# Kernel tuning notes

Hardware: AMD Instinct MI355X
Metric: run time of the kernel (lower is better)

Reference implementation:

```python
import jax, jax.numpy as jnp
import numpy as np

N = 6144   # number of patches (bag size)
L = 1024   # input feature dim
D = 512    # GCN hidden dim
ALPHA = 0.4
THRESH = 0.5


def _layernorm(x, g, b):
    m = jnp.mean(x, axis=-1, keepdims=True)
    v = jnp.mean((x - m) ** 2, axis=-1, keepdims=True)
    return (x - m) / jnp.sqrt(v + 1e-5) * g + b


def _l1rows(x):
    # F.normalize(x, p=1): row-wise L1 normalize with eps=1e-12
    return x / jnp.maximum(jnp.sum(jnp.abs(x), axis=1, keepdims=True), 1e-12)


def _nonlin(x, w1, b1, g, bn, w2, b2):
    h = jax.nn.relu(_layernorm(x @ w1 + b1, g, bn))
    return h @ w2 + b2


def _gcn(x, adj, w, b, g, bn):
    # GraphConvolution: adj @ (x @ W) + bias, then LayerNorm + ReLU
    return jax.nn.relu(_layernorm(adj @ (x @ w) + b, g, bn))


def setup_inputs() -> dict:
    key = jax.random.key(0)
    ks = iter(jax.random.split(key, 64))

    def nrm(shape, s=0.02):
        return jax.random.normal(next(ks), shape, jnp.float32) * s

    inp = {
        'x_path': jax.random.normal(next(ks), (N, L), jnp.float32),
        'maps': jax.random.uniform(next(ks), (N, N), jnp.float32) * 0.1,
    }
    for pre in ['nl0', 'nl1']:
        inp[pre + '_w1'] = nrm((L, D)); inp[pre + '_b1'] = jnp.zeros((D,), jnp.float32)
        inp[pre + '_g'] = jnp.ones((D,), jnp.float32); inp[pre + '_bn'] = jnp.zeros((D,), jnp.float32)
        inp[pre + '_w2'] = nrm((D, D)); inp[pre + '_b2'] = jnp.zeros((D,), jnp.float32)
    for pre in ['gc0', 'gc1', 'gc2', 'ga0', 'ga1', 'ga2']:
        inp[pre + '_w'] = nrm((D, D)); inp[pre + '_b'] = jnp.zeros((D,), jnp.float32)
        inp[pre + '_g'] = jnp.ones((D,), jnp.float32); inp[pre + '_bn'] = jnp.zeros((D,), jnp.float32)
    inp['attn_wa'] = nrm((L, 256)); inp['attn_ba'] = jnp.zeros((256,), jnp.float32)
    inp['attn_wb'] = nrm((L, 256)); inp['attn_bb'] = jnp.zeros((256,), jnp.float32)
    inp['attn_wc'] = nrm((256, 1)); inp['attn_bc'] = jnp.zeros((1,), jnp.float32)
    inp['cls_w'] = nrm((L, 4), 0.001)
    inp['ln_g'] = jnp.ones((L,), jnp.float32); inp['ln_b'] = jnp.zeros((L,), jnp.float32)
    return inp


def reference(x_path, maps,
              nl0_w1, nl0_b1, nl0_g, nl0_bn, nl0_w2, nl0_b2,
              nl1_w1, nl1_b1, nl1_g, nl1_bn, nl1_w2, nl1_b2,
              gc0_w, gc0_b, gc0_g, gc0_bn,
              gc1_w, gc1_b, gc1_g, gc1_bn,
              gc2_w, gc2_b, gc2_g, gc2_bn,
              ga0_w, ga0_b, ga0_g, ga0_bn,
              ga1_w, ga1_b, ga1_g, ga1_bn,
              ga2_w, ga2_b, ga2_g, ga2_bn,
              attn_wa, attn_ba, attn_wb, attn_bb, attn_wc, attn_bc,
              cls_w, ln_g, ln_b):
    # cosine-similarity adjacency: L2-normalize rows, gram matrix, min-max, threshold
    xn = x_path / jnp.maximum(jnp.linalg.norm(x_path, axis=1, keepdims=True), 1e-12)
    cs = xn @ xn.T                                       # [N,N]
    cs = (cs - cs.min()) / (cs.max() - cs.min())
    cs = (cs >= THRESH).astype(jnp.float32)

    # gated attention (eval mode, no dropout): A = Wc (tanh(Wa x) * sigmoid(Wb x))
    a = jnp.tanh(x_path @ attn_wa + attn_ba)
    bg = jax.nn.sigmoid(x_path @ attn_wb + attn_bb)
    agg = (a * bg) @ attn_wc + attn_bc                   # [N,1]

    s = jax.nn.sigmoid(agg)
    aw = s * s.T                                         # outer product [N,N]
    aw = (aw - aw.min()) / (aw.max() - aw.min())
    aw = ALPHA + (1.0 - ALPHA) * aw + maps

    cs = _l1rows(cs)
    aw = _l1rows(aw)

    x0 = _nonlin(x_path, nl0_w1, nl0_b1, nl0_g, nl0_bn, nl0_w2, nl0_b2)
    x1 = _nonlin(x_path, nl1_w1, nl1_b1, nl1_g, nl1_bn, nl1_w2, nl1_b2)

    g1 = _gcn(x0, cs, gc0_w, gc0_b, gc0_g, gc0_bn)
    g1 = _gcn(g1, cs, gc1_w, gc1_b, gc1_g, gc1_bn)
    g1 = _gcn(g1, cs, gc2_w, gc2_b, gc2_g, gc2_bn)

    g2 = _gcn(x1, aw, ga0_w, ga0_b, ga0_g, ga0_bn)
    g2 = _gcn(g2, aw, ga1_w, ga1_b, ga1_g, ga1_bn)
    g2 = _gcn(g2, aw, ga2_w, ga2_b, ga2_g, ga2_bn)

    gcf = jnp.concatenate([g2, g1], axis=1)              # [N, 1024]

    n = x_path.shape[0]
    trans = (cs @ agg) / (n ** 0.5)                      # [N,1]
    fw = jax.nn.softmax(0.3 * trans + 0.7 * agg, axis=0) # softmax over patches
    pooled = fw.T @ gcf                                  # [1, 1024]
    pooled = _layernorm(pooled, ln_g, ln_b)

    logits = pooled @ cls_w                              # [1, 4]
    y_hat = jnp.argmax(logits, axis=1, keepdims=True)    # topk k=1 index
    hazards = jax.nn.sigmoid(logits)
    surv = jnp.cumprod(1.0 - hazards, axis=1)
    return hazards, surv, y_hat
```

## Files before the change

### kernel.cpp

```cpp
#include <hip/hip_runtime.h>

#define N_ 6144
#define L_ 1024
#define D_ 512
#define H_ 256
#define SPARSE_MAX 64u

typedef unsigned short u16;
typedef unsigned long long u64;
typedef __attribute__((ext_vector_type(4))) float f32x4;
typedef __attribute__((ext_vector_type(8))) short s16x8;
typedef __attribute__((ext_vector_type(4))) short s16x4;

__device__ __forceinline__ u16 f2b(float f){
  unsigned u = __float_as_uint(f);
  u += 0x7FFFu + ((u >> 16) & 1u);
  return (u16)(u >> 16);
}
__device__ __forceinline__ float b2f(u16 h){ return __uint_as_float(((unsigned)h) << 16); }
__device__ __forceinline__ unsigned fkey(float f){
  unsigned u = __float_as_uint(f);
  return (u & 0x80000000u) ? ~u : (u | 0x80000000u);
}
__device__ __forceinline__ float funkey(unsigned k){
  unsigned u = (k & 0x80000000u) ? (k & 0x7FFFFFFFu) : ~k;
  return __uint_as_float(u);
}
__device__ __forceinline__ float wave_sum(float v){
  #pragma unroll
  for(int o=32;o;o>>=1) v += __shfl_xor(v,o);
  return v;
}
__device__ __forceinline__ float wave_max(float v){
  #pragma unroll
  for(int o=32;o;o>>=1) v = fmaxf(v,__shfl_xor(v,o));
  return v;
}
__device__ __forceinline__ float wave_min(float v){
  #pragma unroll
  for(int o=32;o;o>>=1) v = fminf(v,__shfl_xor(v,o));
  return v;
}
__device__ __forceinline__ float blk_sum256(float v){
  __shared__ float sm[4];
  v = wave_sum(v);
  __syncthreads();
  if((threadIdx.x&63)==0) sm[threadIdx.x>>6]=v;
  __syncthreads();
  return sm[0]+sm[1]+sm[2]+sm[3];
}
__device__ __forceinline__ float blk_min256(float v){
  __shared__ float sm[4];
  v = wave_min(v);
  __syncthreads();
  if((threadIdx.x&63)==0) sm[threadIdx.x>>6]=v;
  __syncthreads();
  return fminf(fminf(sm[0],sm[1]),fminf(sm[2],sm[3]));
}
__device__ __forceinline__ float blk_max256(float v){
  __shared__ float sm[4];
  v = wave_max(v);
  __syncthreads();
  if((threadIdx.x&63)==0) sm[threadIdx.x>>6]=v;
  __syncthreads();
  return fmaxf(fmaxf(sm[0],sm[1]),fmaxf(sm[2],sm[3]));
}

template<int VW> __device__ __forceinline__ void waitv(){
  if constexpr(VW==8) asm volatile("s_waitcnt vmcnt(8)" ::: "memory");
  else if constexpr(VW==4) asm volatile("s_waitcnt vmcnt(4)" ::: "memory");
  else asm volatile("s_waitcnt vmcnt(0)" ::: "memory");
}

#define STG4(bb,k0) do{ \
  __builtin_amdgcn_global_load_lds((__attribute__((address_space(1))) void*)(gA0+(k0)), (__attribute__((address_space(3))) void*)(lds + (bb)*4096 + (wid<<9)),        16, 0, 0); \
  __builtin_amdgcn_global_load_lds((__attribute__((address_space(1))) void*)(gA1+(k0)), (__attribute__((address_space(3))) void*)(lds + (bb)*4096 + 2048 + (wid<<9)), 16, 0, 0); \
  __builtin_amdgcn_global_load_lds((__attribute__((address_space(1))) void*)(gB0+(k0)), (__attribute__((address_space(3))) void*)(lds + 12288 + (bb)*4096 + (wid<<9)),        16, 0, 0); \
  __builtin_amdgcn_global_load_lds((__attribute__((address_space(1))) void*)(gB1+(k0)), (__attribute__((address_space(3))) void*)(lds + 12288 + (bb)*4096 + 2048 + (wid<<9)), 16, 0, 0); \
}while(0)

template<int MODE>
__global__ __launch_bounds__(256) void gemm_bt(
  const u16* __restrict__ A, const u16* __restrict__ Bt,
  int M, int Nc, int K,
  u16* __restrict__ Cb, unsigned* __restrict__ mmx,
  const unsigned* __restrict__ gate)
{
  if (gate && gate[2] <= SPARSE_MAX) return;
  __shared__ __align__(16) u16 lds[3*4096*2];
  const int tid = threadIdx.x;
  const int wid = tid>>6, lane = tid&63;

  int m0, n0;
  if (MODE==1){
    int t = (int)blockIdx.x;
    t = (t&7)*147 + (t>>3);
    int i=0, rem=t;
    while (rem >= 48-i){ rem -= 48-i; ++i; }
    m0 = i<<7; n0 = (i+rem)<<7;
  } else {
    const int gx = gridDim.x;
    int lid = blockIdx.y*gx + blockIdx.x;
    const int nwg = gx*gridDim.y;
    if ((nwg & 7) == 0) {
      const int chunk = nwg >> 3;
      lid = (lid & 7)*chunk + (lid >> 3);
    }
    m0 = (lid/gx)<<7; n0 = (lid%gx)<<7;
  }
  const int wr = wid>>1, wc = wid&1;

  const int Klen = K / gridDim.z;
  const int kbeg = blockIdx.z * Klen;

  const int srow = (wid<<4) + (lane>>2);
  const int scol = (lane&3)<<3;
  const u16* gA0 = A  + (size_t)(m0+srow   )*K + scol;
  const u16* gA1 = A  + (size_t)(m0+srow+64)*K + scol;
  const u16* gB0 = Bt + (size_t)(n0+srow   )*K + scol;
  const u16* gB1 = Bt + (size_t)(n0+srow+64)*K + scol;

  f32x4 acc[4][4] = {};
  const int lr = lane&15, lk = (lane>>4)<<3;

  const int NIT = Klen>>5;
  STG4(0, kbeg);
  STG4(1, kbeg+32);
  STG4(2, kbeg+64);

  for (int it=0; it<NIT-2; ++it){
    const int b = it - (it/3)*3;
    waitv<8>();
    __builtin_amdgcn_s_barrier();
    const u16* baseA = lds + b*4096;
    const u16* baseB = lds + 12288 + b*4096;
    s16x8 af[4], bfr[4];
    #pragma unroll
    for(int m=0;m<4;m++) af[m]  = *(const s16x8*)(baseA + ((wr<<6)+(m<<4)+lr)*32 + lk);
    #pragma unroll
    for(int n=0;n<4;n++) bfr[n] = *(const s16x8*)(baseB + ((wc<<6)+(n<<4)+lr)*32 + lk);
    asm volatile("s_waitcnt lgkmcnt(0)" ::: "memory");
    __builtin_amdgcn_sched_barrier(0);
    __builtin_amdgcn_s_barrier();
    if (it+3 < NIT) STG4(b, kbeg + ((it+3)<<5));
    #pragma unroll
    for(int m=0;m<4;m++)
      #pragma unroll
      for(int n=0;n<4;n++)
        acc[m][n] = __builtin_amdgcn_mfma_f32_16x16x32_bf16(af[m], bfr[n], acc[m][n], 0,0,0);
  }
  {
    const int it = NIT-2; const int b = it - (it/3)*3;
    waitv<4>();
    __builtin_amdgcn_s_barrier();
    const u16* baseA = lds + b*4096;
    const u16* baseB = lds + 12288 + b*4096;
    s16x8 af[4], bfr[4];
    #pragma unroll
    for(int m=0;m<4;m++) af[m]  = *(const s16x8*)(baseA + ((wr<<6)+(m<<4)+lr)*32 + lk);
    #pragma unroll
    for(int n=0;n<4;n++) bfr[n] = *(const s16x8*)(baseB + ((wc<<6)+(n<<4)+lr)*32 + lk);
    #pragma unroll
    for(int m=0;m<4;m++)
      #pragma unroll
      for(int n=0;n<4;n++)
        acc[m][n] = __builtin_amdgcn_mfma_f32_16x16x32_bf16(af[m], bfr[n], acc[m][n], 0,0,0);
  }
  {
    const int it = NIT-1; const int b = it - (it/3)*3;
    waitv<0>();
    __builtin_amdgcn_s_barrier();
    const u16* baseA = lds + b*4096;
    const u16* baseB = lds + 12288 + b*4096;
    s16x8 af[4], bfr[4];
    #pragma unroll
    for(int m=0;m<4;m++) af[m]  = *(const s16x8*)(baseA + ((wr<<6)+(m<<4)+lr)*32 + lk);
    #pragma unroll
    for(int n=0;n<4;n++) bfr[n] = *(const s16x8*)(baseB + ((wc<<6)+(n<<4)+lr)*32 + lk);
    #pragma unroll
    for(int m=0;m<4;m++)
      #pragma unroll
      for(int n=0;n<4;n++)
        acc[m][n] = __builtin_amdgcn_mfma_f32_16x16x32_bf16(af[m], bfr[n], acc[m][n], 0,0,0);
  }

  float tmin = 3.0e38f, tmax = -3.0e38f;
  if (MODE==1){
    #pragma unroll
    for(int m=0;m<4;m++)
      #pragma unroll
      for(int n=0;n<4;n++){
        f32x4 v = acc[m][n];
        #pragma unroll
        for(int e=0;e<4;e++){ tmin = fminf(tmin,v[e]); tmax = fmaxf(tmax,v[e]); }
      }
  }

  __syncthreads();
  u16* lC = lds;
  {
    const int rb_l = (wr<<6) + ((lane>>4)<<2);
    const int cb_l = (wc<<6) + lr;
    #pragma unroll
    for(int m=0;m<4;m++)
      #pragma unroll
      for(int n=0;n<4;n++){
        f32x4 v = acc[m][n];
        #pragma unroll
        for(int e=0;e<4;e++)
          lC[(rb_l+(m<<4)+e)*128 + cb_l+(n<<4)] = f2b(v[e]);
      }
  }
  __syncthreads();
  u16* Cp = (MODE==0) ? (Cb + (size_t)blockIdx.z * M * Nc) : Cb;
  #pragma unroll
  for(int q=0;q<8;q++){
    int c = (q<<8) + tid;
    int r = c>>4, cc = (c&15)<<3;
    s16x8 v = *(const s16x8*)(lC + r*128 + cc);
    if (MODE==1)
      __builtin_nontemporal_store(v, (s16x8*)(Cp + (size_t)(m0+r)*Nc + n0 + cc));
    else
      *(s16x8*)(Cp + (size_t)(m0+r)*Nc + n0 + cc) = v;
  }

  if (MODE==1){
    tmin = wave_min(tmin); tmax = wave_max(tmax);
    __shared__ float rmn[4], rmx[4];
    if(lane==0){ rmn[wid]=tmin; rmx[wid]=tmax; }
    __syncthreads();
    if(tid==0){
      float mn=fminf(fminf(rmn[0],rmn[1]),fminf(rmn[2],rmn[3]));
      float mx=fmaxf(fmaxf(rmx[0],rmx[1]),fmaxf(rmx[2],rmx[3]));
      atomicMin(mmx+0, fkey(mn));
      atomicMax(mmx+1, fkey(mx));
    }
  }
}

__global__ __launch_bounds__(256) void mirror_lower(u16* __restrict__ C,
  const unsigned* __restrict__ gate)
{
  if (gate[2] <= SPARSE_MAX) return;
  int c0 = blockIdx.x<<5, r0 = blockIdx.y<<5;
  if ((r0>>7) >= (c0>>7)) return;
  __shared__ u16 t[32][33];
  int tx = threadIdx.x&31, ty = threadIdx.x>>5;
  #pragma unroll
  for(int i=0;i<32;i+=8) t[ty+i][tx] = C[(size_t)(r0+ty+i)*N_ + c0+tx];
  __syncthreads();
  #pragma unroll
  for(int i=0;i<32;i+=8)
    __builtin_nontemporal_store(t[tx][ty+i], C + (size_t)(c0+ty+i)*N_ + r0+tx);
}

struct TDesc { const float* src; u16* dst; int R; int C; int base; };
struct TDescs { TDesc d[12]; };
__global__ __launch_bounds__(256) void transpose_cast_multi(TDescs ds, int nd)
{
  int b = (int)blockIdx.x;
  int k = 0;
  for (int q=1;q<nd;q++) if (b >= ds.d[q].base) k = q;
  const float* src = ds.d[k].src;
  u16* dst = ds.d[k].dst;
  int R = ds.d[k].R, C = ds.d[k].C;
  int lt = b - ds.d[k].base;
  int tc = C>>5;
  int bx = lt % tc, by = lt / tc;
  __shared__ float t[32][33];
  int c0 = bx<<5, r0 = by<<5;
  int tx = threadIdx.x&31, ty = threadIdx.x>>5;
  #pragma unroll
  for(int i=0;i<32;i+=8) t[ty+i][tx] = src[(size_t)(r0+ty+i)*C + c0+tx];
  __syncthreads();
  #pragma unroll
  for(int i=0;i<32;i+=8) dst[(size_t)(c0+ty+i)*R + r0+tx] = f2b(t[tx][ty+i]);
}

__global__ __launch_bounds__(256) void transpose_sum_bf(
  const u16* __restrict__ src, size_t pstr, int nsp,
  u16* __restrict__ dst, int R, int C, const unsigned* __restrict__ gate)
{
  if (gate && gate[2] <= SPARSE_MAX) return;
  __shared__ float t[32][33];
  int c0 = blockIdx.x<<5, r0 = blockIdx.y<<5;
  int tx = threadIdx.x&31, ty = threadIdx.x>>5;
  #pragma unroll
  for(int i=0;i<32;i+=8){
    float v = 0;
    for(int p=0;p<nsp;p++)
      v += b2f(src[(size_t)p*pstr + (size_t)(r0+ty+i)*C + c0+tx]);
    t[ty+i][tx] = v;
  }
  __syncthreads();
  #pragma unroll
  for(int i=0;i<32;i+=8) dst[(size_t)(c0+ty+i)*R + r0+tx] = f2b(t[tx][ty+i]);
}

__global__ __launch_bounds__(256) void prep_x(const float* __restrict__ x,
  u16* __restrict__ xb, u16* __restrict__ xnb)
{
  int row = blockIdx.x, t = threadIdx.x;
  const float* p = x + (size_t)row*L_ + (t<<2);
  f32x4 v = *(const f32x4*)p;
  float ss = v[0]*v[0]+v[1]*v[1]+v[2]*v[2]+v[3]*v[3];
  float tot = blk_sum256(ss);
  float inv = 1.0f/fmaxf(sqrtf(tot), 1e-12f);
  u16* pb = xb  + (size_t)row*L_ + (t<<2);
  u16* pn = xnb + (size_t)row*L_ + (t<<2);
  #pragma unroll
  for(int k=0;k<4;k++){ pb[k]=f2b(v[k]); pn[k]=f2b(v[k]*inv); }
}

__global__ __launch_bounds__(256) void attn_epi(const u16* __restrict__ SPA,
  size_t pstr, int nsp,
  const float* __restrict__ ba, const float* __restrict__ bb,
  const float* __restrict__ wc, const float* __restrict__ bc,
  float* __restrict__ agg, float* __restrict__ s)
{
  int row = (blockIdx.x<<2) + (threadIdx.x>>6);
  int lane = threadIdx.x&63;
  float a[4]={0,0,0,0}, b[4]={0,0,0,0};
  for(int p=0;p<nsp;p++){
    s16x4 ua = *(const s16x4*)(SPA + (size_t)p*pstr + (size_t)row*1536 + (lane<<2));
    s16x4 ub = *(const s16x4*)(SPA + (size_t)p*pstr + (size_t)row*1536 + 256 + (lane<<2));
    #pragma unroll
    for(int j=0;j<4;j++){ a[j]+=b2f((u16)ua[j]); b[j]+=b2f((u16)ub[j]); }
  }
  float acc=0;
  #pragma unroll
  for(int j=0;j<4;j++){
    int h = (lane<<2)+j;
    float tv = tanhf(a[j]+ba[h]);
    float sg = 1.0f/(1.0f+expf(-(b[j]+bb[h])));
    acc += tv*sg*wc[h];
  }
  acc = wave_sum(acc);
  if(lane==0){
    float v = acc + bc[0];
    agg[row]=v;
    s[row]=1.0f/(1.0f+expf(-v));
  }
}

__global__ __launch_bounds__(256) void s_stats(const float* __restrict__ s, float* __restrict__ sc){
  int t=threadIdx.x;
  float mn=3e38f, mx=-3e38f;
  for(int i=t;i<N_;i+=256){ float v=s[i]; mn=fminf(mn,v); mx=fmaxf(mx,v); }
  float MN=blk_min256(mn);
  float MX=blk_max256(mx);
  if(t==0){ sc[0]=MN; sc[1]=MX; }
}

__global__ __launch_bounds__(256) void aw_write(const float* __restrict__ maps, const float* __restrict__ s,
  const float* __restrict__ sc, u16* __restrict__ awb)
{
  int i = blockIdx.x, t = threadIdx.x;
  float smin = sc[0], smax = sc[1];
  float mn = smin*smin, mx = smax*smax;
  float beta = 0.6f/(mx-mn);
  float c1 = 0.4f - beta*mn;
  float si = s[i];
  const float* mrow = maps + (size_t)i*N_;
  float mv[24];
  float part = 0;
  #pragma unroll
  for(int q=0;q<24;q++){
    int j = t + (q<<8);
    mv[q] = c1 + beta*si*s[j] + mrow[j];
    part += mv[q];
  }
  float r = blk_sum256(part);
  float inv = 1.0f/fmaxf(r, 1e-12f);
  u16* orow = awb + (size_t)i*N_;
  #pragma unroll
  for(int q=0;q<24;q++)
    __builtin_nontemporal_store(f2b(mv[q]*inv), orow + t + (q<<8));
}

__global__ __launch_bounds__(256) void ln_epi512(const u16* __restrict__ Y, size_t pstr, int nsp,
  int rs, int cbase,
  const float* __restrict__ ki,
  const float* __restrict__ bias, const float* __restrict__ g, const float* __restrict__ bn,
  u16* __restrict__ outb,
  const unsigned* __restrict__ gate)
{
  if (gate && gate[2] <= SPARSE_MAX) return;
  int row = (blockIdx.x<<2)+(threadIdx.x>>6);
  int lane = threadIdx.x&63;
  int c0 = lane<<3;
  float v[8] = {0,0,0,0,0,0,0,0};
  for(int p=0;p<nsp;p++){
    s16x8 u = *(const s16x8*)(Y + (size_t)p*pstr + (size_t)row*rs + cbase + c0);
    #pragma unroll
    for(int j=0;j<8;j++) v[j] += b2f((u16)u[j]);
  }
  float scale = ki ? (1.0f/ki[row]) : 1.0f;
  float sum=0, ssum=0;
  #pragma unroll
  for(int j=0;j<8;j++){ v[j] = v[j]*scale + bias[c0+j]; sum+=v[j]; ssum+=v[j]*v[j]; }
  sum = wave_sum(sum); ssum = wave_sum(ssum);
  float m = sum*(1.0f/D_);
  float var = ssum*(1.0f/D_) - m*m;
  float invsd = rsqrtf(var + 1e-5f);
  u16 ob[8];
  #pragma unroll
  for(int j=0;j<8;j++){
    float o = (v[j]-m)*invsd*g[c0+j] + bn[c0+j];
    o = fmaxf(o, 0.0f);
    ob[j] = f2b(o);
  }
  *(s16x8*)(outb + (size_t)row*D_ + c0) = *(s16x8*)ob;
}

__global__ __launch_bounds__(256) void ln_epi_proj(const u16* __restrict__ Y, size_t pstr, int nsp,
  const float* __restrict__ b1, const float* __restrict__ g1, const float* __restrict__ n1, u16* __restrict__ o1,
  const float* __restrict__ b0, const float* __restrict__ g0, const float* __restrict__ n0, u16* __restrict__ o0)
{
  const int sel = blockIdx.y;
  const int cbase = sel ? 512 : 1024;
  const float* bias = sel ? b0 : b1;
  const float* g    = sel ? g0 : g1;
  const float* bn   = sel ? n0 : n1;
  u16* outb         = sel ? o0 : o1;
  int row = (blockIdx.x<<2)+(threadIdx.x>>6);
  int lane = threadIdx.x&63;
  int c0 = lane<<3;
  float v[8] = {0,0,0,0,0,0,0,0};
  for(int p=0;p<nsp;p++){
    s16x8 u = *(const s16x8*)(Y + (size_t)p*pstr + (size_t)row*1536 + cbase + c0);
    #pragma unroll
    for(int j=0;j<8;j++) v[j] += b2f((u16)u[j]);
  }
  float sum=0, ssum=0;
  #pragma unroll
  for(int j=0;j<8;j++){ v[j] = v[j] + bias[c0+j]; sum+=v[j]; ssum+=v[j]*v[j]; }
  sum = wave_sum(sum); ssum = wave_sum(ssum);
  float m = sum*(1.0f/D_);
  float var = ssum*(1.0f/D_) - m*m;
  float invsd = rsqrtf(var + 1e-5f);
  u16 ob[8];
  #pragma unroll
  for(int j=0;j<8;j++){
    float o = (v[j]-m)*invsd*g[c0+j] + bn[c0+j];
    o = fmaxf(o, 0.0f);
    ob[j] = f2b(o);
  }
  *(s16x8*)(outb + (size_t)row*D_ + c0) = *(s16x8*)ob;
}

__global__ __launch_bounds__(256) void bias_cast(const u16* __restrict__ Y, size_t pstr, int nsp,
  const float* __restrict__ b, u16* __restrict__ outb)
{
  size_t idx = ((size_t)blockIdx.x*256 + threadIdx.x)<<3;
  float v[8] = {0,0,0,0,0,0,0,0};
  for(int p=0;p<nsp;p++){
    s16x8 u = *(const s16x8*)(Y + (size_t)p*pstr + idx);
    #pragma unroll
    for(int j=0;j<8;j++) v[j] += b2f((u16)u[j]);
  }
  int c = (int)(idx & (D_-1));
  u16 ob[8];
  #pragma unroll
  for(int k=0;k<8;k++) ob[k] = f2b(v[k]+b[c+k]);
  *(s16x8*)(outb+idx) = *(s16x8*)ob;
}

__global__ void init_k(unsigned* mmx){
  mmx[0]=0xFFFFFFFFu; mmx[1]=0u; mmx[2]=0u;
}

__global__ __launch_bounds__(256) void binarize_tri(const u16* __restrict__ csb,
  const unsigned* __restrict__ mmx, u64* __restrict__ bm)
{
  int i = blockIdx.x, t = threadIdx.x;
  int lane = t&63, w = t>>6;
  float mn = funkey(mmx[0]), mx = funkey(mmx[1]);
  float th = mn + 0.5f*(mx-mn);
  const u16* row = csb + (size_t)i*N_;
  u64* bmrow = bm + (size_t)i*96;
  const int w0 = i>>6;
  for (int wq = w0 + w; wq < 96; wq += 4){
    int j = (wq<<6) + lane;
    bool on = (j >= i) && (b2f(row[j]) >= th);
    u64 mask = __ballot(on);
    if (lane == 0){
      if (wq == w0) atomicOr((u64*)(bmrow+wq), mask);
      else bmrow[wq] = mask;
    }
    if (on && j > i)
      atomicOr((u64*)(bm + (size_t)j*96 + w0), 1ull << (i&63));
  }
}

__global__ __launch_bounds__(256) void binarize_fin(const u64* __restrict__ bm,
  unsigned* __restrict__ mmx, const float* __restrict__ agg,
  float* __restrict__ ki, float* __restrict__ z)
{
  int i = blockIdx.x, t = threadIdx.x;
  float cnt = 0, dot = 0;
  if (t < 96){
    u64 m = bm[(size_t)i*96 + t];
    cnt = (float)__popcll(m);
    while (m){
      int b = __ffsll((long long)m) - 1;
      m &= m - 1;
      dot += agg[(t<<6) + b];
    }
  }
  float k  = blk_sum256(cnt);
  float dt = blk_sum256(dot);
  if (t==0){
    ki[i] = k;
    float tr = dt/(k*sqrtf((float)N_));
    z[i] = 0.3f*tr + 0.7f*agg[i];
    if (k > (float)SPARSE_MAX)
      atomicMax(mmx+2, (unsigned)(k+0.5f));
  }
}

__global__ __launch_bounds__(256) void binarize_store(u16* __restrict__ csb,
  const unsigned* __restrict__ mmx)
{
  if (mmx[2] <= SPARSE_MAX) return;
  int i = blockIdx.x, t = threadIdx.x;
  float mn = funkey(mmx[0]), mx = funkey(mmx[1]);
  float th = mn + 0.5f*(mx-mn);
  u16* row = csb + (size_t)i*N_;
  #pragma unroll
  for(int q=0;q<24;q++){
    int j = t + (q<<8);
    row[j] = (b2f(row[j]) >= th) ? (u16)0x3F80 : (u16)0;
  }
}

__global__ __launch_bounds__(256) void gather_ln(const u64* __restrict__ bm,
  const u16* __restrict__ SPp, size_t pstr, int nsp,
  const unsigned* __restrict__ gate, const float* __restrict__ ki,
  const float* __restrict__ bias, const float* __restrict__ g, const float* __restrict__ bn,
  u16* __restrict__ outb)
{
  if (gate[2] > SPARSE_MAX) return;
  int i = blockIdx.x, t = threadIdx.x;
  __shared__ u64 wbuf[96];
  __shared__ u16 idx[SPARSE_MAX];
  __shared__ int nn_s;
  if (t < 96) wbuf[t] = bm[(size_t)i*96 + t];
  __syncthreads();
  if (t == 0){
    int nn = 0;
    for(int k=0;k<96;k++){
      u64 m = wbuf[k];
      while(m && nn < (int)SPARSE_MAX){
        int b = __ffsll((long long)m) - 1;
        m &= m - 1;
        idx[nn++] = (u16)((k<<6) + b);
      }
    }
    nn_s = nn;
  }
  __syncthreads();
  int nn = nn_s;
  float a0=0, a1=0;
  for(int k=0;k<nn;k++){
    size_t jb = (size_t)idx[k]*512;
    for(int p=0;p<nsp;p++){
      a0 += b2f(SPp[p*pstr + jb + t]);
      a1 += b2f(SPp[p*pstr + jb + t + 256]);
    }
  }
  float scale = 1.0f/ki[i];
  float v0 = a0*scale + bias[t];
  float v1 = a1*scale + bias[t+256];
  float sum  = blk_sum256(v0+v1);
  float ssum = blk_sum256(v0*v0+v1*v1);
  float m = sum*(1.0f/512.0f);
  float var = ssum*(1.0f/512.0f) - m*m;
  float inv = rsqrtf(var+1e-5f);
  float o0 = fmaxf((v0-m)*inv*g[t]+bn[t], 0.0f);
  float o1 = fmaxf((v1-m)*inv*g[t+256]+bn[t+256], 0.0f);
  outb[(size_t)i*512 + t]       = f2b(o0);
  outb[(size_t)i*512 + t + 256] = f2b(o1);
}

__global__ __launch_bounds__(1024) void softmax_prep(const float* __restrict__ z,
  float* __restrict__ e, float* __restrict__ sexp)
{
  int t = threadIdx.x;
  __shared__ float sm[16];
  float mx=-3e38f;
  for(int i=t;i<N_;i+=1024) mx=fmaxf(mx,z[i]);
  mx = wave_max(mx);
  if((t&63)==0) sm[t>>6]=mx;
  __syncthreads();
  float zm = sm[0];
  #pragma unroll
  for(int w=1;w<16;w++) zm=fmaxf(zm,sm[w]);
  __syncthreads();
  float sum=0;
  for(int i=t;i<N_;i+=1024){ float ee=expf(z[i]-zm); e[i]=ee; sum+=ee; }
  sum = wave_sum(sum);
  if((t&63)==0) sm[t>>6]=sum;
  __syncthreads();
  if(t==0){ float S=0; for(int w=0;w<16;w++) S+=sm[w]; *sexp=S; }
}

__global__ __launch_bounds__(256) void pooled_partial(const float* __restrict__ e,
  const u16* __restrict__ g2b, const u16* __restrict__ g1b, float* __restrict__ part)
{
  int b = blockIdx.x, t = threadIdx.x;
  float a0=0,a1=0,a2=0,a3=0;
  for(int r=0;r<192;r++){
    int row = b*192+r;
    float w = e[row];
    a0 += w * b2f(g2b[(size_t)row*D_ + t]);
    a1 += w * b2f(g2b[(size_t)row*D_ + t+256]);
    a2 += w * b2f(g1b[(size_t)row*D_ + t]);
    a3 += w * b2f(g1b[(size_t)row*D_ + t+256]);
  }
  part[(size_t)b*1024 + t]      = a0;
  part[(size_t)b*1024 + t+256]  = a1;
  part[(size_t)b*1024 + t+512]  = a2;
  part[(size_t)b*1024 + t+768]  = a3;
}

__global__ __launch_bounds__(1024) void final_k(const float* __restrict__ part, const float* __restrict__ sexp,
  const float* __restrict__ lng, const float* __restrict__ lnb,
  const float* __restrict__ clsw, float* __restrict__ out)
{
  int t = threadIdx.x;
  __shared__ float red[16];
  __shared__ float smv[1024];
  __shared__ float lgs[4];
  float p=0;
  for(int b=0;b<32;b++) p += part[b*1024 + t];
  p /= sexp[0];
  float w = wave_sum(p);
  if((t&63)==0) red[t>>6]=w;
  __syncthreads();
  float tot=0;
  #pragma unroll
  for(int i2=0;i2<16;i2++) tot+=red[i2];
  float m = tot*(1.0f/1024.0f);
  __syncthreads();
  float d = p-m;
  w = wave_sum(d*d);
  if((t&63)==0) red[t>>6]=w;
  __syncthreads();
  tot=0;
  #pragma unroll
  for(int i2=0;i2<16;i2++) tot+=red[i2];
  float var = tot*(1.0f/1024.0f);
  float y = d*rsqrtf(var+1e-5f)*lng[t] + lnb[t];
  smv[t]=y;
  __syncthreads();
  if(t<4){
    float lg=0;
    for(int j=0;j<1024;j++) lg += smv[j]*clsw[j*4+t];
    lgs[t]=lg;
  }
  __syncthreads();
  if(t==0){
    float h[4];
    int am=0; float best=lgs[0];
    #pragma unroll
    for(int c2=0;c2<4;c2++){ h[c2]=1.0f/(1.0f+expf(-lgs[c2])); if(lgs[c2]>best){best=lgs[c2];am=c2;} }
    float sv=1.0f;
    #pragma unroll
    for(int c2=0;c2<4;c2++){ out[c2]=h[c2]; sv*=(1.0f-h[c2]); out[4+c2]=sv; }
    out[8]=(float)am;
  }
}

extern "C" void kernel_launch(void* const* d_in, const int* in_sizes, int n_in,
                              void* d_out, int out_size, void* d_ws, size_t ws_size,
                              hipStream_t stream)
{
  const float* x_path =(const float*)d_in[0];
  const float* maps   =(const float*)d_in[1];
  const float* nl0_w1 =(const float*)d_in[2];
  const float* nl0_b1 =(const float*)d_in[3];
  const float* nl0_g  =(const float*)d_in[4];
  const float* nl0_bn =(const float*)d_in[5];
  const float* nl0_w2 =(const float*)d_in[6];
  const float* nl0_b2 =(const float*)d_in[7];
  const float* nl1_w1 =(const float*)d_in[8];
  const float* nl1_b1 =(const float*)d_in[9];
  const float* nl1_g  =(const float*)d_in[10];
  const float* nl1_bn =(const float*)d_in[11];
  const float* nl1_w2 =(const float*)d_in[12];
  const float* nl1_b2 =(const float*)d_in[13];
  const float *gw[6], *gb[6], *gg[6], *gbn[6];
  for(int l=0;l<6;l++){
    gw[l]  = (const float*)d_in[14+l*4+0];
    gb[l]  = (const float*)d_in[14+l*4+1];
    gg[l]  = (const float*)d_in[14+l*4+2];
    gbn[l] = (const float*)d_in[14+l*4+3];
  }
  const float* attn_wa=(const float*)d_in[38];
  const float* attn_ba=(const float*)d_in[39];
  const float* attn_wb=(const float*)d_in[40];
  const float* attn_bb=(const float*)d_in[41];
  const float* attn_wc=(const float*)d_in[42];
  const float* attn_bc=(const float*)d_in[43];
  const float* cls_w  =(const float*)d_in[44];
  const float* ln_g   =(const float*)d_in[45];
  const float* ln_b   =(const float*)d_in[46];

  char* ws=(char*)d_ws;
  size_t off=0;
  auto alc=[&](size_t b)->char*{ char* p=ws+off; off=(off+b+255)&~(size_t)255; return p; };
  u16* BIG = (u16*)alc((size_t)N_*N_*2);
  u16* XB  = (u16*)alc((size_t)N_*L_*2);
  u16* XNB = (u16*)alc((size_t)N_*L_*2);
  u16* WT_proj=(u16*)alc((size_t)1536*L_*2);
  u16* WT_nl0w2=(u16*)alc((size_t)D_*D_*2);
  u16* WT_nl1w2=(u16*)alc((size_t)D_*D_*2);
  u16* WT_g[6];
  for(int l=0;l<6;l++) WT_g[l]=(u16*)alc((size_t)D_*D_*2);
  u16* SP = (u16*)alc((size_t)8*N_*D_*2);
  u16* XWT=(u16*)alc((size_t)D_*N_*2);
  u16* XA0=(u16*)alc((size_t)N_*D_*2);
  u16* XA1=(u16*)alc((size_t)N_*D_*2);
  u16* X0B=(u16*)alc((size_t)N_*D_*2);
  u16* X1B=(u16*)alc((size_t)N_*D_*2);
  u16* YS =(u16*)alc((size_t)N_*D_*2);
  u64* BM =(u64*)alc((size_t)N_*96*8);
  float* PART=(float*)alc((size_t)32*1024*4);
  float* AGG=(float*)alc(N_*4);
  float* SS =(float*)alc(N_*4);
  float* KI =(float*)alc(N_*4);
  float* Z  =(float*)alc(N_*4);
  float* E  =(float*)alc(N_*4);
  float* SC =(float*)alc(256);
  unsigned* MMX=(unsigned*)alc(256);
  float* SEXP=(float*)alc(256);

  const size_t PS_D = (size_t)N_*D_;
  const size_t PS_P = (size_t)N_*1536;

  init_k<<<1,1,0,stream>>>(MMX);
  hipMemsetAsync(BM, 0, (size_t)N_*96*8, stream);
  prep_x<<<N_,256,0,stream>>>(x_path, XB, XNB);

  {
    TDescs ds;
    int base = 0;
    auto add=[&](int k, const float* s, u16* d, int R, int C){
      ds.d[k] = {s, d, R, C, base};
      base += (R>>5)*(C>>5);
    };
    add(0,  attn_wa, WT_proj,                   L_, H_);
    add(1,  attn_wb, WT_proj + (size_t)256*L_,  L_, H_);
    add(2,  nl0_w1,  WT_proj + (size_t)512*L_,  L_, D_);
    add(3,  nl1_w1,  WT_proj + (size_t)1024*L_, L_, D_);
    add(4,  nl0_w2,  WT_nl0w2, D_, D_);
    add(5,  nl1_w2,  WT_nl1w2, D_, D_);
    for(int l=0;l<6;l++) add(6+l, gw[l], WT_g[l], D_, D_);
    transpose_cast_multi<<<base,256,0,stream>>>(ds, 12);
  }

  gemm_bt<0><<<dim3(1536/128, N_/128, 2),256,0,stream>>>(XB, WT_proj, N_, 1536, L_, SP, nullptr, nullptr);
  attn_epi<<<N_/4,256,0,stream>>>(SP, PS_P, 2, attn_ba, attn_bb, attn_wc, attn_bc, AGG, SS);
  s_stats<<<1,256,0,stream>>>(SS,SC);
  aw_write<<<N_,256,0,stream>>>(maps,SS,SC,BIG);

  ln_epi_proj<<<dim3(N_/4,2),256,0,stream>>>(SP,PS_P,2,
    nl1_b1,nl1_g,nl1_bn,XA1, nl0_b1,nl0_g,nl0_bn,XA0);

  gemm_bt<0><<<dim3(D_/128,N_/128,4),256,0,stream>>>(XA1, WT_nl1w2, N_,D_,D_, SP, nullptr, nullptr);
  bias_cast<<<(N_*D_/8)/256,256,0,stream>>>(SP,PS_D,4, nl1_b2, X1B);

  {
    const u16* cur=X1B;
    for(int l=0;l<3;l++){
      int gi = 3+l;
      gemm_bt<0><<<dim3(D_/128,N_/128,4),256,0,stream>>>(cur, WT_g[gi], N_,D_,D_, SP, nullptr, nullptr);
      transpose_sum_bf<<<dim3(D_/32, N_/32),256,0,stream>>>(SP, PS_D, 4, XWT, N_, D_, nullptr);
      gemm_bt<0><<<dim3(D_/128,N_/128,8),256,0,stream>>>(BIG, XWT, N_,D_,N_, SP, nullptr, nullptr);
      u16* nxt = (l==0)? XA1 : (l==1)? YS : X1B;
      ln_epi512<<<N_/4,256,0,stream>>>(SP,PS_D,8, 512,0, nullptr, gb[gi],gg[gi],gbn[gi], nxt, nullptr);
      cur = nxt;
    }
  }

  gemm_bt<0><<<dim3(D_/128,N_/128,4),256,0,stream>>>(XA0, WT_nl0w2, N_,D_,D_, SP, nullptr, nullptr);
  bias_cast<<<(N_*D_/8)/256,256,0,stream>>>(SP,PS_D,4, nl0_b2, X0B);

  gemm_bt<1><<<dim3(1176,1,1),256,0,stream>>>(XNB, XNB, N_,N_,L_, BIG, MMX, nullptr);
  binarize_tri<<<N_,256,0,stream>>>(BIG, MMX, BM);
  binarize_fin<<<N_,256,0,stream>>>(BM, MMX, AGG, KI, Z);
  mirror_lower<<<dim3(N_/32, N_/32),256,0,stream>>>(BIG, MMX);
  binarize_store<<<N_,256,0,stream>>>(BIG, MMX);

  {
    const u16* cur=X0B;
    for(int l=0;l<3;l++){
      int gi = l;
      gemm_bt<0><<<dim3(D_/128,N_/128,4),256,0,stream>>>(cur, WT_g[gi], N_,D_,D_, SP, nullptr, nullptr);
      transpose_sum_bf<<<dim3(D_/32, N_/32),256,0,stream>>>(SP, PS_D, 4, XWT, N_, D_, MMX);
      gemm_bt<0><<<dim3(D_/128,N_/128,8),256,0,stream>>>(BIG, XWT, N_,D_,N_, SP, nullptr, MMX);
      u16* nxt = (l==0)? XA1 : (l==1)? XA0 : X0B;
      gather_ln<<<N_,256,0,stream>>>(BM, SP, PS_D, 4, MMX, KI, gb[gi],gg[gi],gbn[gi], nxt);
      ln_epi512<<<N_/4,256,0,stream>>>(SP,PS_D,8, 512,0, KI, gb[gi],gg[gi],gbn[gi], nxt, MMX);
      cur = nxt;
    }
  }

  softmax_prep<<<1,1024,0,stream>>>(Z,E,SEXP);
  pooled_partial<<<32,256,0,stream>>>(E,X1B,X0B,PART);
  final_k<<<1,1024,0,stream>>>(PART,SEXP,ln_g,ln_b,cls_w,(float*)d_out);

  (void)in_sizes;(void)n_in;(void)out_size;(void)ws_size;
}
```

Before: 768.2 us.

## Use FP8 e4m3 for the aw adjacency GEMMs and cosine-similarity GEMM

```diff
diff --git a/kernel.cpp b/kernel.cpp
--- a/kernel.cpp
+++ b/kernel.cpp
@@ -6,8 +6,10 @@
 #define H_ 256
 #define SPARSE_MAX 64u
 
+typedef unsigned char u8;
 typedef unsigned short u16;
 typedef unsigned long long u64;
+typedef long long i64;
 typedef __attribute__((ext_vector_type(4))) float f32x4;
 typedef __attribute__((ext_vector_type(8))) short s16x8;
 typedef __attribute__((ext_vector_type(4))) short s16x4;
@@ -18,6 +20,23 @@
   return (u16)(u >> 16);
 }
 __device__ __forceinline__ float b2f(u16 h){ return __uint_as_float(((unsigned)h) << 16); }
+__device__ __forceinline__ u8 f2e4(float x){
+  float ax = fabsf(x);
+  u8 s = (x < 0.0f) ? 0x80 : 0;
+  ax = fminf(ax, 448.0f);
+  if (ax < 0.015625f){
+    int m = (int)rintf(ax * 512.0f);
+    return s | (u8)m;
+  }
+  unsigned b = __float_as_uint(ax);
+  int e = (int)(b >> 23) - 127;
+  unsigned mant = b & 0x7FFFFFu;
+  unsigned r = mant + ((1u<<19) - 1u) + ((mant >> 20) & 1u);
+  unsigned mq = r >> 20;
+  if (mq & 8u){ mq = 0; e++; }
+  if (e > 8){ e = 8; mq = 6; }
+  return s | (u8)(((e + 7) << 3) | (mq & 7u));
+}
 __device__ __forceinline__ unsigned fkey(float f){
   unsigned u = __float_as_uint(f);
   return (u & 0x80000000u) ? ~u : (u | 0x80000000u);
@@ -79,15 +98,123 @@
   __builtin_amdgcn_global_load_lds((__attribute__((address_space(1))) void*)(gB1+(k0)), (__attribute__((address_space(3))) void*)(lds + 12288 + (bb)*4096 + 2048 + (wid<<9)), 16, 0, 0); \
 }while(0)
 
-template<int MODE>
 __global__ __launch_bounds__(256) void gemm_bt(
   const u16* __restrict__ A, const u16* __restrict__ Bt,
   int M, int Nc, int K,
-  u16* __restrict__ Cb, unsigned* __restrict__ mmx,
-  const unsigned* __restrict__ gate)
+  u16* __restrict__ Cb, const unsigned* __restrict__ gate)
 {
   if (gate && gate[2] <= SPARSE_MAX) return;
   __shared__ __align__(16) u16 lds[3*4096*2];
+  const int tid = threadIdx.x;
+  const int wid = tid>>6, lane = tid&63;
+
+  const int gx = gridDim.x;
+  int lid = blockIdx.y*gx + blockIdx.x;
+  const int nwg = gx*gridDim.y;
+  if ((nwg & 7) == 0) {
+    const int chunk = nwg >> 3;
+    lid = (lid & 7)*chunk + (lid >> 3);
+  }
+  const int m0 = (lid/gx)<<7, n0 = (lid%gx)<<7;
+  const int wr = wid>>1, wc = wid&1;
+
+  const int Klen = K / gridDim.z;
+  const int kbeg = blockIdx.z * Klen;
+
+  const int srow = (wid<<4) + (lane>>2);
+  const int scol = (lane&3)<<3;
+  const u16* gA0 = A  + (size_t)(m0+srow   )*K + scol;
+  const u16* gA1 = A  + (size_t)(m0+srow+64)*K + scol;
+  const u16* gB0 = Bt + (size_t)(n0+srow   )*K + scol;
+  const u16* gB1 = Bt + (size_t)(n0+srow+64)*K + scol;
+
+  f32x4 acc[4][4] = {};
+  const int lr = lane&15, lk = (lane>>4)<<3;
+
+  const int NIT = Klen>>5;
+  STG4(0, kbeg);
+  STG4(1, kbeg+32);
+  STG4(2, kbeg+64);
+
+  for (int it=0; it<NIT-2; ++it){
+    const int b = it - (it/3)*3;
+    waitv<8>();
+    __builtin_amdgcn_s_barrier();
+    const u16* baseA = lds + b*4096;
+    const u16* baseB = lds + 12288 + b*4096;
+    s16x8 af[4], bfr[4];
+    #pragma unroll
+    for(int m=0;m<4;m++) af[m]  = *(const s16x8*)(baseA + ((wr<<6)+(m<<4)+lr)*32 + lk);
+    #pragma unroll
+    for(int n=0;n<4;n++) bfr[n] = *(const s16x8*)(baseB + ((wc<<6)+(n<<4)+lr)*32 + lk);
+    asm volatile("s_waitcnt lgkmcnt(0)" ::: "memory");
+    __builtin_amdgcn_sched_barrier(0);
+    __builtin_amdgcn_s_barrier();
+    if (it+3 < NIT) STG4(b, kbeg + ((it+3)<<5));
+    #pragma unroll
+    for(int m=0;m<4;m++)
+      #pragma unroll
+      for(int n=0;n<4;n++)
+        acc[m][n] = __builtin_amdgcn_mfma_f32_16x16x32_bf16(af[m], bfr[n], acc[m][n], 0,0,0);
+  }
+  #pragma unroll
+  for (int tail=0; tail<2; ++tail){
+    const int it = NIT-2+tail; const int b = it - (it/3)*3;
+    if (tail==0) waitv<4>(); else waitv<0>();
+    __builtin_amdgcn_s_barrier();
+    const u16* baseA = lds + b*4096;
+    const u16* baseB = lds + 12288 + b*4096;
+    s16x8 af[4], bfr[4];
+    #pragma unroll
+    for(int m=0;m<4;m++) af[m]  = *(const s16x8*)(baseA + ((wr<<6)+(m<<4)+lr)*32 + lk);
+    #pragma unroll
+    for(int n=0;n<4;n++) bfr[n] = *(const s16x8*)(baseB + ((wc<<6)+(n<<4)+lr)*32 + lk);
+    #pragma unroll
+    for(int m=0;m<4;m++)
+      #pragma unroll
+      for(int n=0;n<4;n++)
+        acc[m][n] = __builtin_amdgcn_mfma_f32_16x16x32_bf16(af[m], bfr[n], acc[m][n], 0,0,0);
+  }
+
+  __syncthreads();
+  u16* lC = lds;
+  {
+    const int rb_l = (wr<<6) + ((lane>>4)<<2);
+    const int cb_l = (wc<<6) + lr;
+    #pragma unroll
+    for(int m=0;m<4;m++)
+      #pragma unroll
+      for(int n=0;n<4;n++){
+        f32x4 v = acc[m][n];
+        #pragma unroll
+        for(int e=0;e<4;e++)
+          lC[(rb_l+(m<<4)+e)*128 + cb_l+(n<<4)] = f2b(v[e]);
+      }
+  }
+  __syncthreads();
+  u16* Cp = Cb + (size_t)blockIdx.z * M * Nc;
+  #pragma unroll
+  for(int q=0;q<8;q++){
+    int c = (q<<8) + tid;
+    int r = c>>4, cc = (c&15)<<3;
+    *(s16x8*)(Cp + (size_t)(m0+r)*Nc + n0 + cc) = *(const s16x8*)(lC + r*128 + cc);
+  }
+}
+
+#define STG8(bb,k0) do{ \
+  __builtin_amdgcn_global_load_lds((__attribute__((address_space(1))) void*)(gA0+(k0)),                 (__attribute__((address_space(3))) void*)(lds8 + (bb)*8192 + (wid<<11)),        16, 0, 0); \
+  __builtin_amdgcn_global_load_lds((__attribute__((address_space(1))) void*)(gA0+(size_t)16*K+(k0)),    (__attribute__((address_space(3))) void*)(lds8 + (bb)*8192 + (wid<<11) + 1024), 16, 0, 0); \
+  __builtin_amdgcn_global_load_lds((__attribute__((address_space(1))) void*)(gB0+(k0)),                 (__attribute__((address_space(3))) void*)(lds8 + 24576 + (bb)*8192 + (wid<<11)),        16, 0, 0); \
+  __builtin_amdgcn_global_load_lds((__attribute__((address_space(1))) void*)(gB0+(size_t)16*K+(k0)),    (__attribute__((address_space(3))) void*)(lds8 + 24576 + (bb)*8192 + (wid<<11) + 1024), 16, 0, 0); \
+}while(0)
+
+template<int MODE>
+__global__ __launch_bounds__(256) void gemm_f8(
+  const u8* __restrict__ A, const u8* __restrict__ Bt,
+  int M, int Nc, int K,
+  u16* __restrict__ Cb, unsigned* __restrict__ mmx)
+{
+  __shared__ __align__(16) u8 lds8[3*8192*2];
   const int tid = threadIdx.x;
   const int wid = tid>>6, lane = tid&63;
 
@@ -102,10 +229,7 @@
     const int gx = gridDim.x;
     int lid = blockIdx.y*gx + blockIdx.x;
     const int nwg = gx*gridDim.y;
-    if ((nwg & 7) == 0) {
-      const int chunk = nwg >> 3;
-      lid = (lid & 7)*chunk + (lid >> 3);
-    }
+    if ((nwg & 7) == 0){ const int chunk = nwg>>3; lid = (lid&7)*chunk + (lid>>3); }
     m0 = (lid/gx)<<7; n0 = (lid%gx)<<7;
   }
   const int wr = wid>>1, wc = wid&1;
@@ -113,75 +237,71 @@
   const int Klen = K / gridDim.z;
   const int kbeg = blockIdx.z * Klen;
 
-  const int srow = (wid<<4) + (lane>>2);
-  const int scol = (lane&3)<<3;
-  const u16* gA0 = A  + (size_t)(m0+srow   )*K + scol;
-  const u16* gA1 = A  + (size_t)(m0+srow+64)*K + scol;
-  const u16* gB0 = Bt + (size_t)(n0+srow   )*K + scol;
-  const u16* gB1 = Bt + (size_t)(n0+srow+64)*K + scol;
+  const u8* gA0 = A  + (size_t)(m0 + (wid<<5) + (lane>>2))*K + ((lane&3)<<4);
+  const u8* gB0 = Bt + (size_t)(n0 + (wid<<5) + (lane>>2))*K + ((lane&3)<<4);
 
   f32x4 acc[4][4] = {};
-  const int lr = lane&15, lk = (lane>>4)<<3;
-
-  const int NIT = Klen>>5;
-  STG4(0, kbeg);
-  STG4(1, kbeg+32);
-  STG4(2, kbeg+64);
+  const int lr = lane&15, lk8 = (lane>>4)<<3;
+
+  const int NIT = Klen>>6;
+  STG8(0, kbeg);
+  STG8(1, kbeg+64);
+  STG8(2, kbeg+128);
 
   for (int it=0; it<NIT-2; ++it){
     const int b = it - (it/3)*3;
     waitv<8>();
     __builtin_amdgcn_s_barrier();
-    const u16* baseA = lds + b*4096;
-    const u16* baseB = lds + 12288 + b*4096;
-    s16x8 af[4], bfr[4];
-    #pragma unroll
-    for(int m=0;m<4;m++) af[m]  = *(const s16x8*)(baseA + ((wr<<6)+(m<<4)+lr)*32 + lk);
-    #pragma unroll
-    for(int n=0;n<4;n++) bfr[n] = *(const s16x8*)(baseB + ((wc<<6)+(n<<4)+lr)*32 + lk);
+    const u8* baseA = lds8 + b*8192;
+    const u8* baseB = lds8 + 24576 + b*8192;
+    i64 af[4][2], bfr[4][2];
+    #pragma unroll
+    for(int m=0;m<4;m++){
+      const u8* p = baseA + ((wr<<6)+(m<<4)+lr)*64 + lk8;
+      af[m][0] = *(const i64*)p; af[m][1] = *(const i64*)(p+32);
+    }
+    #pragma unroll
+    for(int n=0;n<4;n++){
+      const u8* p = baseB + ((wc<<6)+(n<<4)+lr)*64 + lk8;
+      bfr[n][0] = *(const i64*)p; bfr[n][1] = *(const i64*)(p+32);
+    }
     asm volatile("s_waitcnt lgkmcnt(0)" ::: "memory");
     __builtin_amdgcn_sched_barrier(0);
     __builtin_amdgcn_s_barrier();
-    if (it+3 < NIT) STG4(b, kbeg + ((it+3)<<5));
+    if (it+3 < NIT) STG8(b, kbeg + ((it+3)<<6));
     #pragma unroll
     for(int m=0;m<4;m++)
       #pragma unroll
-      for(int n=0;n<4;n++)
-        acc[m][n] = __builtin_amdgcn_mfma_f32_16x16x32_bf16(af[m], bfr[n], acc[m][n], 0,0,0);
-  }
-  {
-    const int it = NIT-2; const int b = it - (it/3)*3;
-    waitv<4>();
+      for(int n=0;n<4;n++){
+        acc[m][n] = __builtin_amdgcn_mfma_f32_16x16x32_fp8_fp8(af[m][0], bfr[n][0], acc[m][n], 0,0,0);
+        acc[m][n] = __builtin_amdgcn_mfma_f32_16x16x32_fp8_fp8(af[m][1], bfr[n][1], acc[m][n], 0,0,0);
+      }
+  }
+  #pragma unroll
+  for (int tail=0; tail<2; ++tail){
+    const int it = NIT-2+tail; const int b = it - (it/3)*3;
+    if (tail==0) waitv<4>(); else waitv<0>();
     __builtin_amdgcn_s_barrier();
-    const u16* baseA = lds + b*4096;
-    const u16* baseB = lds + 12288 + b*4096;
-    s16x8 af[4], bfr[4];
-    #pragma unroll
-    for(int m=0;m<4;m++) af[m]  = *(const s16x8*)(baseA + ((wr<<6)+(m<<4)+lr)*32 + lk);
-    #pragma unroll
-    for(int n=0;n<4;n++) bfr[n] = *(const s16x8*)(baseB + ((wc<<6)+(n<<4)+lr)*32 + lk);
+    const u8* baseA = lds8 + b*8192;
+    const u8* baseB = lds8 + 24576 + b*8192;
+    i64 af[4][2], bfr[4][2];
+    #pragma unroll
+    for(int m=0;m<4;m++){
+      const u8* p = baseA + ((wr<<6)+(m<<4)+lr)*64 + lk8;
+      af[m][0] = *(const i64*)p; af[m][1] = *(const i64*)(p+32);
+    }
+    #pragma unroll
+    for(int n=0;n<4;n++){
+      const u8* p = baseB + ((wc<<6)+(n<<4)+lr)*64 + lk8;
+      bfr[n][0] = *(const i64*)p; bfr[n][1] = *(const i64*)(p+32);
+    }
     #pragma unroll
     for(int m=0;m<4;m++)
       #pragma unroll
-      for(int n=0;n<4;n++)
-        acc[m][n] = __builtin_amdgcn_mfma_f32_16x16x32_bf16(af[m], bfr[n], acc[m][n], 0,0,0);
-  }
-  {
-    const int it = NIT-1; const int b = it - (it/3)*3;
-    waitv<0>();
-    __builtin_amdgcn_s_barrier();
-    const u16* baseA = lds + b*4096;
-    const u16* baseB = lds + 12288 + b*4096;
-    s16x8 af[4], bfr[4];
-    #pragma unroll
-    for(int m=0;m<4;m++) af[m]  = *(const s16x8*)(baseA + ((wr<<6)+(m<<4)+lr)*32 + lk);
-    #pragma unroll
-    for(int n=0;n<4;n++) bfr[n] = *(const s16x8*)(baseB + ((wc<<6)+(n<<4)+lr)*32 + lk);
-    #pragma unroll
-    for(int m=0;m<4;m++)
-      #pragma unroll
-      for(int n=0;n<4;n++)
-        acc[m][n] = __builtin_amdgcn_mfma_f32_16x16x32_bf16(af[m], bfr[n], acc[m][n], 0,0,0);
+      for(int n=0;n<4;n++){
+        acc[m][n] = __builtin_amdgcn_mfma_f32_16x16x32_fp8_fp8(af[m][0], bfr[n][0], acc[m][n], 0,0,0);
+        acc[m][n] = __builtin_amdgcn_mfma_f32_16x16x32_fp8_fp8(af[m][1], bfr[n][1], acc[m][n], 0,0,0);
+      }
   }
 
   float tmin = 3.0e38f, tmax = -3.0e38f;
@@ -197,7 +317,7 @@
   }
 
   __syncthreads();
-  u16* lC = lds;
+  u16* lC = (u16*)lds8;
   {
     const int rb_l = (wr<<6) + ((lane>>4)<<2);
     const int cb_l = (wc<<6) + lr;
@@ -297,19 +417,40 @@
   for(int i=0;i<32;i+=8) dst[(size_t)(c0+ty+i)*R + r0+tx] = f2b(t[tx][ty+i]);
 }
 
+__global__ __launch_bounds__(256) void transpose_sum_f8(
+  const u16* __restrict__ src, size_t pstr, int nsp,
+  u8* __restrict__ dst, int R, int C)
+{
+  __shared__ float t[32][33];
+  int c0 = blockIdx.x<<5, r0 = blockIdx.y<<5;
+  int tx = threadIdx.x&31, ty = threadIdx.x>>5;
+  #pragma unroll
+  for(int i=0;i<32;i+=8){
+    float v = 0;
+    for(int p=0;p<nsp;p++)
+      v += b2f(src[(size_t)p*pstr + (size_t)(r0+ty+i)*C + c0+tx]);
+    t[ty+i][tx] = v;
+  }
+  __syncthreads();
+  #pragma unroll
+  for(int i=0;i<32;i+=8) dst[(size_t)(c0+ty+i)*R + r0+tx] = f2e4(t[tx][ty+i] * 4.0f);
+}
+
 __global__ __launch_bounds__(256) void prep_x(const float* __restrict__ x,
-  u16* __restrict__ xb, u16* __restrict__ xnb)
+  u16* __restrict__ xb, u8* __restrict__ xn8)
 {
   int row = blockIdx.x, t = threadIdx.x;
   const float* p = x + (size_t)row*L_ + (t<<2);
   f32x4 v = *(const f32x4*)p;
   float ss = v[0]*v[0]+v[1]*v[1]+v[2]*v[2]+v[3]*v[3];
   float tot = blk_sum256(ss);
-  float inv = 1.0f/fmaxf(sqrtf(tot), 1e-12f);
-  u16* pb = xb  + (size_t)row*L_ + (t<<2);
-  u16* pn = xnb + (size_t)row*L_ + (t<<2);
-  #pragma unroll
-  for(int k=0;k<4;k++){ pb[k]=f2b(v[k]); pn[k]=f2b(v[k]*inv); }
+  float inv = 16.0f/fmaxf(sqrtf(tot), 1e-12f);
+  u16* pb = xb + (size_t)row*L_ + (t<<2);
+  u16 ob[4]; u8 o8[4];
+  #pragma unroll
+  for(int k=0;k<4;k++){ ob[k]=f2b(v[k]); o8[k]=f2e4(v[k]*inv); }
+  *(s16x4*)pb = *(s16x4*)ob;
+  *(unsigned*)(xn8 + (size_t)row*L_ + (t<<2)) = *(unsigned*)o8;
 }
 
 __global__ __launch_bounds__(256) void attn_epi(const u16* __restrict__ SPA,
@@ -353,7 +494,7 @@
 }
 
 __global__ __launch_bounds__(256) void aw_write(const float* __restrict__ maps, const float* __restrict__ s,
-  const float* __restrict__ sc, u16* __restrict__ awb)
+  const float* __restrict__ sc, u8* __restrict__ aw8)
 {
   int i = blockIdx.x, t = threadIdx.x;
   float smin = sc[0], smax = sc[1];
@@ -362,24 +503,30 @@
   float c1 = 0.4f - beta*mn;
   float si = s[i];
   const float* mrow = maps + (size_t)i*N_;
-  float mv[24];
+  float mv[6][4];
   float part = 0;
   #pragma unroll
-  for(int q=0;q<24;q++){
-    int j = t + (q<<8);
-    mv[q] = c1 + beta*si*s[j] + mrow[j];
-    part += mv[q];
+  for(int q=0;q<6;q++){
+    int j = (t<<2) + (q<<10);
+    f32x4 mm = *(const f32x4*)(mrow + j);
+    f32x4 sv = *(const f32x4*)(s + j);
+    #pragma unroll
+    for(int e=0;e<4;e++){ mv[q][e] = c1 + beta*si*sv[e] + mm[e]; part += mv[q][e]; }
   }
   float r = blk_sum256(part);
-  float inv = 1.0f/fmaxf(r, 1e-12f);
-  u16* orow = awb + (size_t)i*N_;
-  #pragma unroll
-  for(int q=0;q<24;q++)
-    __builtin_nontemporal_store(f2b(mv[q]*inv), orow + t + (q<<8));
+  float inv = 2048.0f/fmaxf(r, 1e-12f);
+  u8* orow = aw8 + (size_t)i*N_;
+  #pragma unroll
+  for(int q=0;q<6;q++){
+    u8 o[4];
+    #pragma unroll
+    for(int e=0;e<4;e++) o[e] = f2e4(mv[q][e]*inv);
+    __builtin_nontemporal_store(*(unsigned*)o, (unsigned*)(orow + (t<<2) + (q<<10)));
+  }
 }
 
 __global__ __launch_bounds__(256) void ln_epi512(const u16* __restrict__ Y, size_t pstr, int nsp,
-  int rs, int cbase,
+  int rs, int cbase, float dsc,
   const float* __restrict__ ki,
   const float* __restrict__ bias, const float* __restrict__ g, const float* __restrict__ bn,
   u16* __restrict__ outb,
@@ -395,7 +542,7 @@
     #pragma unroll
     for(int j=0;j<8;j++) v[j] += b2f((u16)u[j]);
   }
-  float scale = ki ? (1.0f/ki[row]) : 1.0f;
+  float scale = dsc * (ki ? (1.0f/ki[row]) : 1.0f);
   float sum=0, ssum=0;
   #pragma unroll
   for(int j=0;j<8;j++){ v[j] = v[j]*scale + bias[c0+j]; sum+=v[j]; ssum+=v[j]*v[j]; }
@@ -712,7 +859,7 @@
   auto alc=[&](size_t b)->char*{ char* p=ws+off; off=(off+b+255)&~(size_t)255; return p; };
   u16* BIG = (u16*)alc((size_t)N_*N_*2);
   u16* XB  = (u16*)alc((size_t)N_*L_*2);
-  u16* XNB = (u16*)alc((size_t)N_*L_*2);
+  u8*  XN8 = (u8*) alc((size_t)N_*L_);
   u16* WT_proj=(u16*)alc((size_t)1536*L_*2);
   u16* WT_nl0w2=(u16*)alc((size_t)D_*D_*2);
   u16* WT_nl1w2=(u16*)alc((size_t)D_*D_*2);
@@ -720,6 +867,7 @@
   for(int l=0;l<6;l++) WT_g[l]=(u16*)alc((size_t)D_*D_*2);
   u16* SP = (u16*)alc((size_t)8*N_*D_*2);
   u16* XWT=(u16*)alc((size_t)D_*N_*2);
+  u8*  XWT8=(u8*)alc((size_t)D_*N_);
   u16* XA0=(u16*)alc((size_t)N_*D_*2);
   u16* XA1=(u16*)alc((size_t)N_*D_*2);
   u16* X0B=(u16*)alc((size_t)N_*D_*2);
@@ -738,10 +886,11 @@
 
   const size_t PS_D = (size_t)N_*D_;
   const size_t PS_P = (size_t)N_*1536;
+  u8* AW8 = (u8*)BIG;
 
   init_k<<<1,1,0,stream>>>(MMX);
   hipMemsetAsync(BM, 0, (size_t)N_*96*8, stream);
-  prep_x<<<N_,256,0,stream>>>(x_path, XB, XNB);
+  prep_x<<<N_,256,0,stream>>>(x_path, XB, XN8);
 
   {
     TDescs ds;
@@ -760,34 +909,34 @@
     transpose_cast_multi<<<base,256,0,stream>>>(ds, 12);
   }
 
-  gemm_bt<0><<<dim3(1536/128, N_/128, 2),256,0,stream>>>(XB, WT_proj, N_, 1536, L_, SP, nullptr, nullptr);
+  gemm_bt<<<dim3(1536/128, N_/128, 2),256,0,stream>>>(XB, WT_proj, N_, 1536, L_, SP, nullptr);
   attn_epi<<<N_/4,256,0,stream>>>(SP, PS_P, 2, attn_ba, attn_bb, attn_wc, attn_bc, AGG, SS);
   s_stats<<<1,256,0,stream>>>(SS,SC);
-  aw_write<<<N_,256,0,stream>>>(maps,SS,SC,BIG);
+  aw_write<<<N_,256,0,stream>>>(maps,SS,SC,AW8);
 
   ln_epi_proj<<<dim3(N_/4,2),256,0,stream>>>(SP,PS_P,2,
     nl1_b1,nl1_g,nl1_bn,XA1, nl0_b1,nl0_g,nl0_bn,XA0);
 
-  gemm_bt<0><<<dim3(D_/128,N_/128,4),256,0,stream>>>(XA1, WT_nl1w2, N_,D_,D_, SP, nullptr, nullptr);
+  gemm_bt<<<dim3(D_/128,N_/128,4),256,0,stream>>>(XA1, WT_nl1w2, N_,D_,D_, SP, nullptr);
   bias_cast<<<(N_*D_/8)/256,256,0,stream>>>(SP,PS_D,4, nl1_b2, X1B);
 
   {
     const u16* cur=X1B;
     for(int l=0;l<3;l++){
       int gi = 3+l;
-      gemm_bt<0><<<dim3(D_/128,N_/128,4),256,0,stream>>>(cur, WT_g[gi], N_,D_,D_, SP, nullptr, nullptr);
-      transpose_sum_bf<<<dim3(D_/32, N_/32),256,0,stream>>>(SP, PS_D, 4, XWT, N_, D_, nullptr);
-      gemm_bt<0><<<dim3(D_/128,N_/128,8),256,0,stream>>>(BIG, XWT, N_,D_,N_, SP, nullptr, nullptr);
+      gemm_bt<<<dim3(D_/128,N_/128,4),256,0,stream>>>(cur, WT_g[gi], N_,D_,D_, SP, nullptr);
+      transpose_sum_f8<<<dim3(D_/32, N_/32),256,0,stream>>>(SP, PS_D, 4, XWT8, N_, D_);
+      gemm_f8<0><<<dim3(D_/128,N_/128,8),256,0,stream>>>(AW8, XWT8, N_,D_,N_, SP, nullptr);
       u16* nxt = (l==0)? XA1 : (l==1)? YS : X1B;
-      ln_epi512<<<N_/4,256,0,stream>>>(SP,PS_D,8, 512,0, nullptr, gb[gi],gg[gi],gbn[gi], nxt, nullptr);
+      ln_epi512<<<N_/4,256,0,stream>>>(SP,PS_D,8, 512,0, 1.0f/8192.0f, nullptr, gb[gi],gg[gi],gbn[gi], nxt, nullptr);
       cur = nxt;
     }
   }
 
-  gemm_bt<0><<<dim3(D_/128,N_/128,4),256,0,stream>>>(XA0, WT_nl0w2, N_,D_,D_, SP, nullptr, nullptr);
+  gemm_bt<<<dim3(D_/128,N_/128,4),256,0,stream>>>(XA0, WT_nl0w2, N_,D_,D_, SP, nullptr);
   bias_cast<<<(N_*D_/8)/256,256,0,stream>>>(SP,PS_D,4, nl0_b2, X0B);
 
-  gemm_bt<1><<<dim3(1176,1,1),256,0,stream>>>(XNB, XNB, N_,N_,L_, BIG, MMX, nullptr);
+  gemm_f8<1><<<dim3(1176,1,1),256,0,stream>>>(XN8, XN8, N_,N_,L_, BIG, MMX);
   binarize_tri<<<N_,256,0,stream>>>(BIG, MMX, BM);
   binarize_fin<<<N_,256,0,stream>>>(BM, MMX, AGG, KI, Z);
   mirror_lower<<<dim3(N_/32, N_/32),256,0,stream>>>(BIG, MMX);
@@ -797,12 +946,12 @@
     const u16* cur=X0B;
     for(int l=0;l<3;l++){
       int gi = l;
-      gemm_bt<0><<<dim3(D_/128,N_/128,4),256,0,stream>>>(cur, WT_g[gi], N_,D_,D_, SP, nullptr, nullptr);
+      gemm_bt<<<dim3(D_/128,N_/128,4),256,0,stream>>>(cur, WT_g[gi], N_,D_,D_, SP, nullptr);
       transpose_sum_bf<<<dim3(D_/32, N_/32),256,0,stream>>>(SP, PS_D, 4, XWT, N_, D_, MMX);
-      gemm_bt<0><<<dim3(D_/128,N_/128,8),256,0,stream>>>(BIG, XWT, N_,D_,N_, SP, nullptr, MMX);
+      gemm_bt<<<dim3(D_/128,N_/128,8),256,0,stream>>>(BIG, XWT, N_,D_,N_, SP, MMX);
       u16* nxt = (l==0)? XA1 : (l==1)? XA0 : X0B;
       gather_ln<<<N_,256,0,stream>>>(BM, SP, PS_D, 4, MMX, KI, gb[gi],gg[gi],gbn[gi], nxt);
-      ln_epi512<<<N_/4,256,0,stream>>>(SP,PS_D,8, 512,0, KI, gb[gi],gg[gi],gbn[gi], nxt, MMX);
+      ln_epi512<<<N_/4,256,0,stream>>>(SP,PS_D,8, 512,0, 1.0f, KI, gb[gi],gg[gi],gbn[gi], nxt, MMX);
       cur = nxt;
     }
   }
```

Measured after the change: 852.1 us. 1.11x slower.
